# Optimization experiments

Hardware: AMD Instinct MI355X
Metric: run time of the kernel (lower is better)

Reference implementation:

```python
import jax, jax.numpy as jnp
import numpy as np
import math

EMBED = 768
HEADS = 12
HEAD_DIM = EMBED // HEADS

def setup_inputs() -> dict:
    key = jax.random.key(0)
    ks = jax.random.split(key, 9)
    B, T, C = 32, 1024, EMBED
    s = 1.0 / math.sqrt(C)
    return {
        "hidden_states": jax.random.normal(ks[0], (B, T, C), dtype=jnp.float32),
        "q_w": jax.random.normal(ks[1], (C, C), dtype=jnp.float32) * s,
        "q_b": jnp.zeros((C,), dtype=jnp.float32),
        "k_w": jax.random.normal(ks[2], (C, C), dtype=jnp.float32) * s,
        "k_b": jnp.zeros((C,), dtype=jnp.float32),
        "v_w": jax.random.normal(ks[3], (C, C), dtype=jnp.float32) * s,
        "v_b": jnp.zeros((C,), dtype=jnp.float32),
        "o_w": jax.random.normal(ks[4], (C, C), dtype=jnp.float32) * s,
        "o_b": jnp.zeros((C,), dtype=jnp.float32),
    }

def reference(hidden_states, q_w, q_b, k_w, k_b, v_w, v_b, o_w, o_b):
    B, T, C = hidden_states.shape
    H, D = HEADS, C // HEADS
    # Linear: x @ W^T + b (torch nn.Linear convention); here weights stored (C, C)
    q = (hidden_states @ q_w.T + q_b).reshape(B, T, H, D).transpose(0, 2, 1, 3)
    k = (hidden_states @ k_w.T + k_b).reshape(B, T, H, D).transpose(0, 2, 1, 3)
    v = (hidden_states @ v_w.T + v_b).reshape(B, T, H, D).transpose(0, 2, 1, 3)
    scale = 1.0 / math.sqrt(D)
    scores = jnp.einsum("bhqd,bhkd->bhqk", q, k) * scale
    attn = jax.nn.softmax(scores, axis=-1)
    out = jnp.einsum("bhqk,bhkd->bhqd", attn, v)  # (B,H,T,D)
    out = out.transpose(0, 2, 1, 3).reshape(B, T, C)
    return out @ o_w.T + o_b
```

## Files before the change

kernel.cpp:

```cpp
#include <hip/hip_runtime.h>
#include <hip/hip_bf16.h>

#define B_ 32
#define T_ 1024
#define C_ 768
#define H_ 12
#define D_ 64
#define BT_ (B_*T_)
#define CC_ (C_*C_)

typedef __attribute__((ext_vector_type(4))) float f32x4;
typedef __attribute__((ext_vector_type(8))) short bf16x8;
typedef __attribute__((ext_vector_type(4))) short short4_t;
typedef __attribute__((ext_vector_type(2))) unsigned int u32x2;
typedef unsigned short u16;
typedef unsigned int u32;

#define QSCALE 0.1803368801111244f

__device__ __forceinline__ float bf2f(u16 u){
  union { float f; unsigned int i; } v; v.i = ((unsigned int)u)<<16; return v.f;
}
__device__ __forceinline__ u16 f2bf(float f){
  union { float f; unsigned int i; } v; v.f = f;
  return (u16)((v.i + 0x7fffu + ((v.i>>16)&1u)) >> 16);
}
__device__ __forceinline__ u32 pack2bf(float lo, float hi){
  union { float f; u32 i; } a, b; a.f = lo; b.f = hi;
  return ((a.i + 0x8000u) >> 16) | ((b.i + 0x8000u) & 0xFFFF0000u);
}
__device__ __forceinline__ void split2(float f, u16& h, u16& l){
  h = f2bf(f);
  l = f2bf(f - bf2f(h));
}

__device__ __forceinline__ void gll16(const void* g, void* l){
  __builtin_amdgcn_global_load_lds(
      (const __attribute__((address_space(1))) u32*)g,
      (__attribute__((address_space(3))) u32*)l, 16, 0, 0);
}

__global__ void sentinel_kernel(float* out, int n){
  int i = blockIdx.x*blockDim.x + threadIdx.x;
  if (i < n) out[i] = 12345.0f;
}

__global__ void xquant_kernel(const float* __restrict__ x, u16* __restrict__ xb, int n8){
  int i = blockIdx.x*blockDim.x + threadIdx.x;
  int stride = gridDim.x*blockDim.x;
  for (; i < n8; i += stride) {
    f32x4 a = *(const f32x4*)(x + (size_t)i*8);
    f32x4 b = *(const f32x4*)(x + (size_t)i*8 + 4);
    bf16x8 o;
    #pragma unroll
    for (int j = 0; j < 4; ++j) { o[j] = (short)f2bf(a[j]); o[j+4] = (short)f2bf(b[j]); }
    *(bf16x8*)(xb + (size_t)i*8) = o;
  }
}

__global__ void wquant_kernel(const float* __restrict__ qw, const float* __restrict__ kw,
                              const float* __restrict__ vw, const float* __restrict__ ow,
                              u16* __restrict__ W3b, u16* __restrict__ Wohi,
                              u16* __restrict__ Wolo){
  int i = (blockIdx.x*blockDim.x + threadIdx.x)*4;
  if (i >= CC_) return;
  f32x4 q = *(const f32x4*)(qw+i);
  f32x4 k = *(const f32x4*)(kw+i);
  f32x4 v = *(const f32x4*)(vw+i);
  f32x4 o = *(const f32x4*)(ow+i);
  short4_t tq, tk, tv, th, tl;
  #pragma unroll
  for (int j = 0; j < 4; ++j) {
    tq[j] = (short)f2bf(q[j]);
    tk[j] = (short)f2bf(k[j]);
    tv[j] = (short)f2bf(v[j]);
    u16 hh, ll; split2(o[j], hh, ll);
    th[j] = (short)hh; tl[j] = (short)ll;
  }
  *(short4_t*)(W3b + i)          = tq;
  *(short4_t*)(W3b + CC_ + i)    = tk;
  *(short4_t*)(W3b + 2*CC_ + i)  = tv;
  *(short4_t*)(Wohi + i)         = th;
  *(short4_t*)(Wolo + i)         = tl;
}

__global__ __launch_bounds__(512,1)
void gemm_qkv(const u16* __restrict__ Ab, const u16* __restrict__ Wb,
              const float* __restrict__ bq, const float* __restrict__ bk,
              const float* __restrict__ bv,
              u16* __restrict__ Qb, u16* __restrict__ Kb, u16* __restrict__ Vb)
{
  __shared__ __align__(1024) u16 sA[2][256*64];
  __shared__ __align__(1024) u16 sB[2][256*64];
  const int tid = threadIdx.x;
  const int lane = tid & 63;
  const int l15 = lane & 15, l16 = lane >> 4;
  const int wave = tid >> 6;
  const int wm = wave >> 2, wn = wave & 3;
  const int bid = blockIdx.x;
  const int xcd = bid & 7;
  const int idx = bid >> 3;
  const int mloc = idx / 9, nb = idx % 9;
  const int m0 = (xcd*16 + mloc) * 256;
  const int n0 = nb * 256;
  const int z  = nb / 3;
  const float* bias = (z==0) ? bq : (z==1 ? bk : bv);

  const int lrow = lane >> 3;
  const int cbyte = ((lane & 7) ^ lrow) << 4;

  f32x4 acc[8][4];
  #pragma unroll
  for (int i=0;i<8;++i)
    #pragma unroll
    for (int j=0;j<4;++j)
      acc[i][j] = (f32x4){0.f,0.f,0.f,0.f};

  auto stageA = [&](int c, int kt){
    #pragma unroll
    for (int i=0;i<4;++i){
      int row = i*64 + wave*8 + lrow;
      gll16((const char*)(Ab + (size_t)(m0+row)*C_ + kt*64) + cbyte,
            sA[c] + (i*64 + wave*8)*64);
    }
  };
  auto stageB = [&](int c, int kt){
    #pragma unroll
    for (int i=0;i<4;++i){
      int row = i*64 + wave*8 + lrow;
      gll16((const char*)(Wb + (size_t)(n0+row)*C_ + kt*64) + cbyte,
            sB[c] + (i*64 + wave*8)*64);
    }
  };

  stageA(0,0); stageB(0,0);
  asm volatile("s_waitcnt vmcnt(0)" ::: "memory");
  __syncthreads();

  for (int t = 0; t < 12; ++t) {
    const int c = t & 1;
    const u16* Atile = sA[c];
    const u16* Btile = sB[c];
    bf16x8 aLo[4][2], aHi[4][2], bLo[2][2], bHi[2][2];

    if (t < 11) stageA(c^1, t+1);
    #pragma unroll
    for (int mf=0; mf<4; ++mf)
      #pragma unroll
      for (int kc=0; kc<2; ++kc){
        int row = wm*128 + mf*16 + l15;
        aLo[mf][kc] = *(const bf16x8*)((const char*)Atile + row*128 + ((kc*64 + l16*16) ^ ((row&7)<<4)));
      }
    #pragma unroll
    for (int nf=0; nf<2; ++nf)
      #pragma unroll
      for (int kc=0; kc<2; ++kc){
        int row = wn*64 + nf*16 + l15;
        bLo[nf][kc] = *(const bf16x8*)((const char*)Btile + row*128 + ((kc*64 + l16*16) ^ ((row&7)<<4)));
      }
    __builtin_amdgcn_s_setprio(1);
    #pragma unroll
    for (int mf=0; mf<4; ++mf)
      #pragma unroll
      for (int nf=0; nf<2; ++nf)
        #pragma unroll
        for (int kc=0; kc<2; ++kc)
          acc[mf][nf] = __builtin_amdgcn_mfma_f32_16x16x32_bf16(aLo[mf][kc], bLo[nf][kc], acc[mf][nf],0,0,0);
    __builtin_amdgcn_s_setprio(0);

    if (t < 11) stageB(c^1, t+1);
    #pragma unroll
    for (int nf=0; nf<2; ++nf)
      #pragma unroll
      for (int kc=0; kc<2; ++kc){
        int row = wn*64 + (nf+2)*16 + l15;
        bHi[nf][kc] = *(const bf16x8*)((const char*)Btile + row*128 + ((kc*64 + l16*16) ^ ((row&7)<<4)));
      }
    __builtin_amdgcn_s_setprio(1);
    #pragma unroll
    for (int mf=0; mf<4; ++mf)
      #pragma unroll
      for (int nf=0; nf<2; ++nf)
        #pragma unroll
        for (int kc=0; kc<2; ++kc)
          acc[mf][nf+2] = __builtin_amdgcn_mfma_f32_16x16x32_bf16(aLo[mf][kc], bHi[nf][kc], acc[mf][nf+2],0,0,0);
    __builtin_amdgcn_s_setprio(0);

    #pragma unroll
    for (int mf=0; mf<4; ++mf)
      #pragma unroll
      for (int kc=0; kc<2; ++kc){
        int row = wm*128 + (mf+4)*16 + l15;
        aHi[mf][kc] = *(const bf16x8*)((const char*)Atile + row*128 + ((kc*64 + l16*16) ^ ((row&7)<<4)));
      }
    __builtin_amdgcn_s_setprio(1);
    #pragma unroll
    for (int mf=0; mf<4; ++mf)
      #pragma unroll
      for (int nf=0; nf<2; ++nf)
        #pragma unroll
        for (int kc=0; kc<2; ++kc)
          acc[mf+4][nf+2] = __builtin_amdgcn_mfma_f32_16x16x32_bf16(aHi[mf][kc], bHi[nf][kc], acc[mf+4][nf+2],0,0,0);
    __builtin_amdgcn_s_setprio(0);

    __builtin_amdgcn_s_setprio(1);
    #pragma unroll
    for (int mf=0; mf<4; ++mf)
      #pragma unroll
      for (int nf=0; nf<2; ++nf)
        #pragma unroll
        for (int kc=0; kc<2; ++kc)
          acc[mf+4][nf] = __builtin_amdgcn_mfma_f32_16x16x32_bf16(aHi[mf][kc], bLo[nf][kc], acc[mf+4][nf],0,0,0);
    __builtin_amdgcn_s_setprio(0);
    if (t < 11) {
      asm volatile("s_waitcnt vmcnt(0)" ::: "memory");
      __syncthreads();
    }
  }

  #pragma unroll
  for (int mf = 0; mf < 8; ++mf) {
    #pragma unroll
    for (int nf = 0; nf < 4; ++nf) {
      int mgb = m0 + wm*128 + mf*16 + l16*4;
      int ngz = (nb%3)*256 + wn*64 + nf*16 + l15;
      float bv = bias[ngz];
      int b = mgb >> 10, t0 = mgb & 1023;
      int h = ngz >> 6, d = ngz & 63;
      int bh_ = b*H_ + h;
      if (z == 2) {
        short4_t vh;
        #pragma unroll
        for (int r = 0; r < 4; ++r)
          vh[r] = (short)f2bf(acc[mf][nf][r] + bv);
        size_t idx2 = ((size_t)bh_*D_ + d)*T_ + t0;
        *(short4_t*)&Vb[idx2] = vh;
      } else {
        u16* dst = (z==0) ? Qb : Kb;
        float scale = (z==0) ? QSCALE : 1.0f;
        #pragma unroll
        for (int r = 0; r < 4; ++r) {
          size_t idx2 = ((size_t)bh_*T_ + (t0+r))*D_ + d;
          dst[idx2] = f2bf((acc[mf][nf][r] + bv) * scale);
        }
      }
    }
  }
}

__global__ __launch_bounds__(256,2)
void gemm_out(const u16* __restrict__ Ab, const u16* __restrict__ Whi,
              const u16* __restrict__ Wlo_, const float* __restrict__ bo,
              float* __restrict__ Out)
{
  __shared__ __align__(1024) u16 sA[128*64];
  __shared__ __align__(1024) u16 sB[128*64];
  __shared__ __align__(1024) u16 sBl[128*64];
  const int tid = threadIdx.x;
  const int lane = tid & 63;
  const int l15 = lane & 15, l16 = lane >> 4;
  const int wave = tid >> 6;
  const int wr = wave >> 1, wc = wave & 1;

  const int bid = blockIdx.x;
  const int xcd = bid & 7;
  const int idx = bid >> 3;
  const int nb = idx % 6, mloc = idx / 6;
  const int m0 = (xcd*32 + mloc) * 128;
  const int n0 = nb * 128;

  const int lrow = lane >> 3;
  const int cbyte = ((lane & 7) ^ lrow) << 4;

  f32x4 acc[4][4];
  #pragma unroll
  for (int i=0;i<4;++i)
    #pragma unroll
    for (int j=0;j<4;++j)
      acc[i][j] = (f32x4){0.f,0.f,0.f,0.f};

  for (int k0 = 0; k0 < C_; k0 += 64) {
    __syncthreads();
    #pragma unroll
    for (int sg = 0; sg < 4; ++sg) {
      int seg = wave*4 + sg;
      int row = seg*8 + lrow;
      gll16((const char*)(Ab   + (size_t)(m0+row)*C_ + k0) + cbyte, sA  + seg*512);
      gll16((const char*)(Whi  + (size_t)(n0+row)*C_ + k0) + cbyte, sB  + seg*512);
      gll16((const char*)(Wlo_ + (size_t)(n0+row)*C_ + k0) + cbyte, sBl + seg*512);
    }
    asm volatile("s_waitcnt vmcnt(0)" ::: "memory");
    __syncthreads();

    #pragma unroll
    for (int kc = 0; kc < 2; ++kc) {
      bf16x8 a[4], bh[4], bl[4];
      #pragma unroll
      for (int mf = 0; mf < 4; ++mf) {
        int row = wr*64 + mf*16 + l15;
        int off = (row<<7) + ((kc*64 + l16*16) ^ ((row&7)<<4));
        a[mf] = *(const bf16x8*)((const char*)sA + off);
      }
      #pragma unroll
      for (int nf = 0; nf < 4; ++nf) {
        int row = wc*64 + nf*16 + l15;
        int off = (row<<7) + ((kc*64 + l16*16) ^ ((row&7)<<4));
        bh[nf] = *(const bf16x8*)((const char*)sB + off);
        bl[nf] = *(const bf16x8*)((const char*)sBl + off);
      }
      #pragma unroll
      for (int mf = 0; mf < 4; ++mf)
        #pragma unroll
        for (int nf = 0; nf < 4; ++nf) {
          acc[mf][nf] = __builtin_amdgcn_mfma_f32_16x16x32_bf16(a[mf], bh[nf], acc[mf][nf],0,0,0);
          acc[mf][nf] = __builtin_amdgcn_mfma_f32_16x16x32_bf16(a[mf], bl[nf], acc[mf][nf],0,0,0);
        }
    }
  }

  #pragma unroll
  for (int mf = 0; mf < 4; ++mf) {
    #pragma unroll
    for (int nf = 0; nf < 4; ++nf) {
      int mgb = m0 + wr*64 + mf*16 + l16*4;
      int ng  = n0 + wc*64 + nf*16 + l15;
      float bv = bo[ng];
      #pragma unroll
      for (int r = 0; r < 4; ++r)
        Out[(size_t)(mgb+r)*C_ + ng] = acc[mf][nf][r] + bv;
    }
  }
}

__global__ __launch_bounds__(256,2)
void attn_kernel(const u16* __restrict__ Qb, const u16* __restrict__ Kb,
                 const u16* __restrict__ Vb, u16* __restrict__ AOb)
{
  __shared__ __align__(16) u16 sK[64*64];
  __shared__ __align__(16) u16 sV[64*64];
  __shared__ __align__(16) u32 sP[4][32*32];
  const int tid = threadIdx.x;
  const int lane = tid & 63;
  const int l15 = lane & 15, l16 = lane >> 4;
  const int wave = tid >> 6;
  const int bid = blockIdx.x;
  const int sw  = (bid & 7) * 384 + (bid >> 3);
  const int bh  = sw >> 3;
  const int q0  = (sw & 7) * 128 + wave * 32;

  bf16x8 qh[2][2];
  #pragma unroll
  for (int mf = 0; mf < 2; ++mf)
    #pragma unroll
    for (int kc = 0; kc < 2; ++kc)
      qh[mf][kc] = *(const bf16x8*)(Qb + ((size_t)bh*T_ + q0 + mf*16 + l15)*D_ + kc*32 + l16*8);

  f32x4 o[2][4];
  #pragma unroll
  for (int mf = 0; mf < 2; ++mf)
    #pragma unroll
    for (int i = 0; i < 4; ++i) o[mf][i] = (f32x4){0.f,0.f,0.f,0.f};
  float l_r[2] = {0.f, 0.f};

  const size_t kbase = (size_t)bh * (T_*D_);
  const size_t vbase = (size_t)bh * (D_*T_);
  u32* pw = sP[wave];

  int srow[2], sdst[2], scolb[2];
  #pragma unroll
  for (int iss = 0; iss < 2; ++iss) {
    int oo = (iss*256 + tid)*16;
    srow[iss]  = oo >> 7;
    scolb[iss] = oo & 127;
    sdst[iss]  = (srow[iss]<<7) | (scolb[iss] ^ ((srow[iss]&7)<<4));
  }
  bf16x8 kreg[2], vreg[2];
  #pragma unroll
  for (int iss = 0; iss < 2; ++iss) {
    kreg[iss] = *(const bf16x8*)((const char*)(Kb + kbase + (size_t)srow[iss]*D_) + scolb[iss]);
    vreg[iss] = *(const bf16x8*)((const char*)(Vb + vbase + (size_t)srow[iss]*T_) + scolb[iss]);
  }

  for (int kt = 0; kt < T_/64; ++kt) {
    __syncthreads();
    #pragma unroll
    for (int iss = 0; iss < 2; ++iss) {
      *(bf16x8*)((char*)sK + sdst[iss]) = kreg[iss];
      *(bf16x8*)((char*)sV + sdst[iss]) = vreg[iss];
    }
    if (kt + 1 < T_/64) {
      #pragma unroll
      for (int iss = 0; iss < 2; ++iss) {
        kreg[iss] = *(const bf16x8*)((const char*)(Kb + kbase + (size_t)((kt+1)*64+srow[iss])*D_) + scolb[iss]);
        vreg[iss] = *(const bf16x8*)((const char*)(Vb + vbase + (size_t)srow[iss]*T_ + (kt+1)*64) + scolb[iss]);
      }
    }
    __syncthreads();

    f32x4 s[2][4];
    #pragma unroll
    for (int mf = 0; mf < 2; ++mf)
      #pragma unroll
      for (int nf = 0; nf < 4; ++nf) s[mf][nf] = (f32x4){0.f,0.f,0.f,0.f};
    __builtin_amdgcn_s_setprio(1);
    #pragma unroll
    for (int nf = 0; nf < 4; ++nf) {
      #pragma unroll
      for (int kc = 0; kc < 2; ++kc) {
        int row = nf*16 + l15;
        int off = (row<<7) | (((kc*64) + l16*16) ^ ((row&7)<<4));
        bf16x8 kf = *(const bf16x8*)((const char*)sK + off);
        s[0][nf] = __builtin_amdgcn_mfma_f32_16x16x32_bf16(kf, qh[0][kc], s[0][nf],0,0,0);
        s[1][nf] = __builtin_amdgcn_mfma_f32_16x16x32_bf16(kf, qh[1][kc], s[1][nf],0,0,0);
      }
    }
    __builtin_amdgcn_s_setprio(0);

    #pragma unroll
    for (int mf = 0; mf < 2; ++mf) {
      int q = mf*16 + l15;
      u32* prow = pw + q*32;
      int swz = (q & 7) << 2;
      #pragma unroll
      for (int nf = 0; nf < 4; ++nf) {
        float p0 = __builtin_amdgcn_exp2f(s[mf][nf][0]);
        float p1 = __builtin_amdgcn_exp2f(s[mf][nf][1]);
        float p2 = __builtin_amdgcn_exp2f(s[mf][nf][2]);
        float p3 = __builtin_amdgcn_exp2f(s[mf][nf][3]);
        l_r[mf] += (p0 + p1) + (p2 + p3);
        u32x2 w2;
        w2[0] = pack2bf(p0, p1);
        w2[1] = pack2bf(p2, p3);
        *(u32x2*)(prow + ((8*nf + 2*l16) ^ swz)) = w2;
      }
    }

    __builtin_amdgcn_s_setprio(1);
    #pragma unroll
    for (int kc = 0; kc < 2; ++kc) {
      bf16x8 pf[2];
      #pragma unroll
      for (int mf = 0; mf < 2; ++mf) {
        int q = mf*16 + l15;
        pf[mf] = *(const bf16x8*)(pw + q*32 + ((kc*16 + l16*4) ^ ((q&7)<<2)));
      }
      #pragma unroll
      for (int df = 0; df < 4; ++df) {
        int row = df*16 + l15;
        int offv = (row<<7) | (((kc*64) + l16*16) ^ ((row&7)<<4));
        bf16x8 vf = *(const bf16x8*)((const char*)sV + offv);
        o[0][df] = __builtin_amdgcn_mfma_f32_16x16x32_bf16(pf[0], vf, o[0][df],0,0,0);
        o[1][df] = __builtin_amdgcn_mfma_f32_16x16x32_bf16(pf[1], vf, o[1][df],0,0,0);
      }
    }
    __builtin_amdgcn_s_setprio(0);
  }

  #pragma unroll
  for (int mf = 0; mf < 2; ++mf) {
    float t = l_r[mf];
    t += __shfl_xor(t, 16);
    t += __shfl_xor(t, 32);
    l_r[mf] = t;
  }

  const int b = bh / H_, h = bh % H_;
  #pragma unroll
  for (int mf = 0; mf < 2; ++mf)
    #pragma unroll
    for (int r = 0; r < 4; ++r) {
      float inv = 1.0f / __shfl(l_r[mf], (l16 << 2) + r);
      int t = q0 + mf*16 + l16*4 + r;
      size_t rowb = ((size_t)(b*T_ + t))*C_ + h*D_;
      #pragma unroll
      for (int df = 0; df < 4; ++df)
        AOb[rowb + df*16 + l15] = f2bf(o[mf][df][r] * inv);
    }
}

extern "C" void kernel_launch(void* const* d_in, const int* in_sizes, int n_in,
                              void* d_out, int out_size, void* d_ws, size_t ws_size,
                              hipStream_t stream) {
  const float* X  = (const float*)d_in[0];
  const float* qw = (const float*)d_in[1];
  const float* qb = (const float*)d_in[2];
  const float* kw = (const float*)d_in[3];
  const float* kb = (const float*)d_in[4];
  const float* vw = (const float*)d_in[5];
  const float* vb = (const float*)d_in[6];
  const float* ow = (const float*)d_in[7];
  const float* ob = (const float*)d_in[8];
  float* out = (float*)d_out;

  const size_t SZ = (size_t)BT_*C_*sizeof(u16);
  const size_t NEED = 4*SZ + 5*(size_t)CC_*sizeof(u16);
  if (ws_size < NEED) {
    sentinel_kernel<<<(out_size+255)/256,256,0,stream>>>(out, out_size);
    return;
  }
  char* ws = (char*)d_ws;
  u16* Qb   = (u16*)(ws + 0*SZ);
  u16* Kb   = (u16*)(ws + 1*SZ);
  u16* Vb   = (u16*)(ws + 2*SZ);
  u16* AOb  = (u16*)(ws + 3*SZ);
  u16* W3b  = (u16*)(ws + 4*SZ);
  u16* Wohi = W3b + 3*(size_t)CC_;
  u16* Wolo = Wohi + (size_t)CC_;
  u16* Xb   = AOb;

  wquant_kernel<<<CC_/4/256,256,0,stream>>>(qw, kw, vw, ow, W3b, Wohi, Wolo);
  xquant_kernel<<<2048,256,0,stream>>>(X, Xb, BT_*C_/8);
  gemm_qkv<<<1152,512,0,stream>>>(Xb, W3b, qb, kb, vb, Qb, Kb, Vb);
  attn_kernel<<<3072,256,0,stream>>>(Qb, Kb, Vb, AOb);
  gemm_out<<<1536,256,0,stream>>>(AOb, Wohi, Wolo, ob, out);
}
```

Before: 390.0 us.

## Deepen QKV GEMM prefetch pipeline and drop hi/lo split for output weights

The QKV GEMM now loads each stage in half-tiles and issues them two iterations ahead. Partial vmcnt waits and raw s_barrier calls inside the compute phases replace the full wait plus __syncthreads at the end of each iteration, so global loads overlap more of the MFMA work. Separately, the output projection weights are kept as a single bf16 copy instead of a hi/lo pair, which halves the MFMAs and weight traffic in gemm_out. The cost is lower precision for the output projection, and the finer barrier scheme makes the shared-memory buffer reuse more delicate.

Result: faster. 373.4 us (-4.3%).

```diff
diff --git a/kernel.cpp b/kernel.cpp
--- a/kernel.cpp
+++ b/kernel.cpp
@@ -29,10 +29,6 @@
   union { float f; u32 i; } a, b; a.f = lo; b.f = hi;
   return ((a.i + 0x8000u) >> 16) | ((b.i + 0x8000u) & 0xFFFF0000u);
 }
-__device__ __forceinline__ void split2(float f, u16& h, u16& l){
-  h = f2bf(f);
-  l = f2bf(f - bf2f(h));
-}
 
 __device__ __forceinline__ void gll16(const void* g, void* l){
   __builtin_amdgcn_global_load_lds(
@@ -60,28 +56,25 @@
 
 __global__ void wquant_kernel(const float* __restrict__ qw, const float* __restrict__ kw,
                               const float* __restrict__ vw, const float* __restrict__ ow,
-                              u16* __restrict__ W3b, u16* __restrict__ Wohi,
-                              u16* __restrict__ Wolo){
+                              u16* __restrict__ W3b, u16* __restrict__ Wob){
   int i = (blockIdx.x*blockDim.x + threadIdx.x)*4;
   if (i >= CC_) return;
   f32x4 q = *(const f32x4*)(qw+i);
   f32x4 k = *(const f32x4*)(kw+i);
   f32x4 v = *(const f32x4*)(vw+i);
   f32x4 o = *(const f32x4*)(ow+i);
-  short4_t tq, tk, tv, th, tl;
+  short4_t tq, tk, tv, to;
   #pragma unroll
   for (int j = 0; j < 4; ++j) {
     tq[j] = (short)f2bf(q[j]);
     tk[j] = (short)f2bf(k[j]);
     tv[j] = (short)f2bf(v[j]);
-    u16 hh, ll; split2(o[j], hh, ll);
-    th[j] = (short)hh; tl[j] = (short)ll;
+    to[j] = (short)f2bf(o[j]);
   }
   *(short4_t*)(W3b + i)          = tq;
   *(short4_t*)(W3b + CC_ + i)    = tk;
   *(short4_t*)(W3b + 2*CC_ + i)  = tv;
-  *(short4_t*)(Wohi + i)         = th;
-  *(short4_t*)(Wolo + i)         = tl;
+  *(short4_t*)(Wob + i)          = to;
 }
 
 __global__ __launch_bounds__(512,1)
@@ -116,26 +109,27 @@
     for (int j=0;j<4;++j)
       acc[i][j] = (f32x4){0.f,0.f,0.f,0.f};
 
-  auto stageA = [&](int c, int kt){
-    #pragma unroll
-    for (int i=0;i<4;++i){
-      int row = i*64 + wave*8 + lrow;
-      gll16((const char*)(Ab + (size_t)(m0+row)*C_ + kt*64) + cbyte,
-            sA[c] + (i*64 + wave*8)*64);
+  auto stA = [&](int c, int kt, int h){
+    #pragma unroll
+    for (int i=0;i<2;++i){
+      int rl = h*128 + i*64 + wave*8;
+      gll16((const char*)(Ab + (size_t)(m0+rl+lrow)*C_ + kt*64) + cbyte,
+            sA[c] + (size_t)rl*64);
     }
   };
-  auto stageB = [&](int c, int kt){
-    #pragma unroll
-    for (int i=0;i<4;++i){
-      int row = i*64 + wave*8 + lrow;
-      gll16((const char*)(Wb + (size_t)(n0+row)*C_ + kt*64) + cbyte,
-            sB[c] + (i*64 + wave*8)*64);
+  auto stB = [&](int c, int kt, int h){
+    #pragma unroll
+    for (int i=0;i<2;++i){
+      int rl = h*128 + i*64 + wave*8;
+      gll16((const char*)(Wb + (size_t)(n0+rl+lrow)*C_ + kt*64) + cbyte,
+            sB[c] + (size_t)rl*64);
     }
   };
 
-  stageA(0,0); stageB(0,0);
-  asm volatile("s_waitcnt vmcnt(0)" ::: "memory");
-  __syncthreads();
+  stA(0,0,0); stB(0,0,0); stB(0,0,1); stA(0,0,1);
+  stA(1,1,0); stB(1,1,0); stB(1,1,1);
+  asm volatile("s_waitcnt vmcnt(6)" ::: "memory");
+  __builtin_amdgcn_s_barrier();
 
   for (int t = 0; t < 12; ++t) {
     const int c = t & 1;
@@ -143,7 +137,7 @@
     const u16* Btile = sB[c];
     bf16x8 aLo[4][2], aHi[4][2], bLo[2][2], bHi[2][2];
 
-    if (t < 11) stageA(c^1, t+1);
+    if (t+1 < 12) stA(c^1, t+1, 1);
     #pragma unroll
     for (int mf=0; mf<4; ++mf)
       #pragma unroll
@@ -158,6 +152,9 @@
         int row = wn*64 + nf*16 + l15;
         bLo[nf][kc] = *(const bf16x8*)((const char*)Btile + row*128 + ((kc*64 + l16*16) ^ ((row&7)<<4)));
       }
+    asm volatile("" ::: "memory");
+    __builtin_amdgcn_s_barrier();
+    asm volatile("s_waitcnt lgkmcnt(0)" ::: "memory");
     __builtin_amdgcn_s_setprio(1);
     #pragma unroll
     for (int mf=0; mf<4; ++mf)
@@ -167,8 +164,9 @@
         for (int kc=0; kc<2; ++kc)
           acc[mf][nf] = __builtin_amdgcn_mfma_f32_16x16x32_bf16(aLo[mf][kc], bLo[nf][kc], acc[mf][nf],0,0,0);
     __builtin_amdgcn_s_setprio(0);
-
-    if (t < 11) stageB(c^1, t+1);
+    asm volatile("" ::: "memory");
+    __builtin_amdgcn_s_barrier();
+
     #pragma unroll
     for (int nf=0; nf<2; ++nf)
       #pragma unroll
@@ -176,6 +174,9 @@
         int row = wn*64 + (nf+2)*16 + l15;
         bHi[nf][kc] = *(const bf16x8*)((const char*)Btile + row*128 + ((kc*64 + l16*16) ^ ((row&7)<<4)));
       }
+    asm volatile("" ::: "memory");
+    __builtin_amdgcn_s_barrier();
+    asm volatile("s_waitcnt lgkmcnt(0)" ::: "memory");
     __builtin_amdgcn_s_setprio(1);
     #pragma unroll
     for (int mf=0; mf<4; ++mf)
@@ -185,7 +186,10 @@
         for (int kc=0; kc<2; ++kc)
           acc[mf][nf+2] = __builtin_amdgcn_mfma_f32_16x16x32_bf16(aLo[mf][kc], bHi[nf][kc], acc[mf][nf+2],0,0,0);
     __builtin_amdgcn_s_setprio(0);
-
+    asm volatile("" ::: "memory");
+    __builtin_amdgcn_s_barrier();
+
+    if (t+2 < 12) stB(c, t+2, 0);
     #pragma unroll
     for (int mf=0; mf<4; ++mf)
       #pragma unroll
@@ -193,6 +197,9 @@
         int row = wm*128 + (mf+4)*16 + l15;
         aHi[mf][kc] = *(const bf16x8*)((const char*)Atile + row*128 + ((kc*64 + l16*16) ^ ((row&7)<<4)));
       }
+    asm volatile("" ::: "memory");
+    __builtin_amdgcn_s_barrier();
+    asm volatile("s_waitcnt lgkmcnt(0)" ::: "memory");
     __builtin_amdgcn_s_setprio(1);
     #pragma unroll
     for (int mf=0; mf<4; ++mf)
@@ -202,7 +209,10 @@
         for (int kc=0; kc<2; ++kc)
           acc[mf+4][nf+2] = __builtin_amdgcn_mfma_f32_16x16x32_bf16(aHi[mf][kc], bHi[nf][kc], acc[mf+4][nf+2],0,0,0);
     __builtin_amdgcn_s_setprio(0);
-
+    asm volatile("" ::: "memory");
+    __builtin_amdgcn_s_barrier();
+
+    if (t+2 < 12) { stB(c, t+2, 1); stA(c, t+2, 0); }
     __builtin_amdgcn_s_setprio(1);
     #pragma unroll
     for (int mf=0; mf<4; ++mf)
@@ -212,10 +222,9 @@
         for (int kc=0; kc<2; ++kc)
           acc[mf+4][nf] = __builtin_amdgcn_mfma_f32_16x16x32_bf16(aHi[mf][kc], bLo[nf][kc], acc[mf+4][nf],0,0,0);
     __builtin_amdgcn_s_setprio(0);
-    if (t < 11) {
-      asm volatile("s_waitcnt vmcnt(0)" ::: "memory");
-      __syncthreads();
-    }
+    if (t < 10)      asm volatile("s_waitcnt vmcnt(6)" ::: "memory");
+    else if (t == 10) asm volatile("s_waitcnt vmcnt(0)" ::: "memory");
+    if (t < 11) __builtin_amdgcn_s_barrier();
   }
 
   #pragma unroll
@@ -249,13 +258,11 @@
 }
 
 __global__ __launch_bounds__(256,2)
-void gemm_out(const u16* __restrict__ Ab, const u16* __restrict__ Whi,
-              const u16* __restrict__ Wlo_, const float* __restrict__ bo,
-              float* __restrict__ Out)
+void gemm_out(const u16* __restrict__ Ab, const u16* __restrict__ Wb,
+              const float* __restrict__ bo, float* __restrict__ Out)
 {
   __shared__ __align__(1024) u16 sA[128*64];
   __shared__ __align__(1024) u16 sB[128*64];
-  __shared__ __align__(1024) u16 sBl[128*64];
   const int tid = threadIdx.x;
   const int lane = tid & 63;
   const int l15 = lane & 15, l16 = lane >> 4;
@@ -285,16 +292,15 @@
     for (int sg = 0; sg < 4; ++sg) {
       int seg = wave*4 + sg;
       int row = seg*8 + lrow;
-      gll16((const char*)(Ab   + (size_t)(m0+row)*C_ + k0) + cbyte, sA  + seg*512);
-      gll16((const char*)(Whi  + (size_t)(n0+row)*C_ + k0) + cbyte, sB  + seg*512);
-      gll16((const char*)(Wlo_ + (size_t)(n0+row)*C_ + k0) + cbyte, sBl + seg*512);
+      gll16((const char*)(Ab + (size_t)(m0+row)*C_ + k0) + cbyte, sA + seg*512);
+      gll16((const char*)(Wb + (size_t)(n0+row)*C_ + k0) + cbyte, sB + seg*512);
     }
     asm volatile("s_waitcnt vmcnt(0)" ::: "memory");
     __syncthreads();
 
     #pragma unroll
     for (int kc = 0; kc < 2; ++kc) {
-      bf16x8 a[4], bh[4], bl[4];
+      bf16x8 a[4], bh[4];
       #pragma unroll
       for (int mf = 0; mf < 4; ++mf) {
         int row = wr*64 + mf*16 + l15;
@@ -306,15 +312,12 @@
         int row = wc*64 + nf*16 + l15;
         int off = (row<<7) + ((kc*64 + l16*16) ^ ((row&7)<<4));
         bh[nf] = *(const bf16x8*)((const char*)sB + off);
-        bl[nf] = *(const bf16x8*)((const char*)sBl + off);
       }
       #pragma unroll
       for (int mf = 0; mf < 4; ++mf)
         #pragma unroll
-        for (int nf = 0; nf < 4; ++nf) {
+        for (int nf = 0; nf < 4; ++nf)
           acc[mf][nf] = __builtin_amdgcn_mfma_f32_16x16x32_bf16(a[mf], bh[nf], acc[mf][nf],0,0,0);
-          acc[mf][nf] = __builtin_amdgcn_mfma_f32_16x16x32_bf16(a[mf], bl[nf], acc[mf][nf],0,0,0);
-        }
     }
   }
 
@@ -493,7 +496,7 @@
   float* out = (float*)d_out;
 
   const size_t SZ = (size_t)BT_*C_*sizeof(u16);
-  const size_t NEED = 4*SZ + 5*(size_t)CC_*sizeof(u16);
+  const size_t NEED = 4*SZ + 4*(size_t)CC_*sizeof(u16);
   if (ws_size < NEED) {
     sentinel_kernel<<<(out_size+255)/256,256,0,stream>>>(out, out_size);
     return;
@@ -504,13 +507,12 @@
   u16* Vb   = (u16*)(ws + 2*SZ);
   u16* AOb  = (u16*)(ws + 3*SZ);
   u16* W3b  = (u16*)(ws + 4*SZ);
-  u16* Wohi = W3b + 3*(size_t)CC_;
-  u16* Wolo = Wohi + (size_t)CC_;
+  u16* Wob  = W3b + 3*(size_t)CC_;
   u16* Xb   = AOb;
 
-  wquant_kernel<<<CC_/4/256,256,0,stream>>>(qw, kw, vw, ow, W3b, Wohi, Wolo);
+  wquant_kernel<<<CC_/4/256,256,0,stream>>>(qw, kw, vw, ow, W3b, Wob);
   xquant_kernel<<<2048,256,0,stream>>>(X, Xb, BT_*C_/8);
   gemm_qkv<<<1152,512,0,stream>>>(Xb, W3b, qb, kb, vb, Qb, Kb, Vb);
   attn_kernel<<<3072,256,0,stream>>>(Qb, Kb, Vb, AOb);
-  gemm_out<<<1536,256,0,stream>>>(AOb, Wohi, Wolo, ob, out);
-}
+  gemm_out<<<1536,256,0,stream>>>(AOb, Wob, ob, out);
+}
```
